# Kernel optimization log

Measured on AMD Instinct MI355X. Metric: run time of the kernel, lower is better.

## Reference

```python
import jax, jax.numpy as jnp
import numpy as np

E = 500000          # num edges
N = 50000           # num nodes
D_IN = 32           # n_input_features (edge feature dim)
D_HID = 128         # n_hidden_features
D_NODE = 16         # n_node_features; MLP head outputs D_NODE**2


def _linear_params(key, d_in, d_out):
    kw, kb = jax.random.split(key)
    bound = 1.0 / np.sqrt(d_in)
    W = jax.random.uniform(kw, (d_out, d_in), jnp.float32, -bound, bound)
    b = jax.random.uniform(kb, (d_out,), jnp.float32, -bound, bound)
    return W, b


def setup_inputs() -> dict:
    key = jax.random.key(0)
    k1, k2, k3, k4, k5, k6, k7 = jax.random.split(key, 7)
    edge_features = jax.random.normal(k1, (E, D_IN), jnp.float32)
    node_features = jax.random.normal(k2, (N, D_NODE), jnp.float32)
    edge_index = jax.random.randint(k3, (E, 2), 0, N, jnp.int64 if jax.config.jax_enable_x64 else jnp.int32)
    W1, b1 = _linear_params(k4, D_IN, D_HID)
    W2, b2 = _linear_params(k5, D_HID, D_HID)
    W3, b3 = _linear_params(k6, D_HID, D_HID)
    W4, b4 = _linear_params(k7, D_HID, D_NODE * D_NODE)
    return {
        "edge_features": edge_features,
        "node_features": node_features,
        "W1": W1, "b1": b1, "W2": W2, "b2": b2,
        "W3": W3, "b3": b3, "W4": W4, "b4": b4,
        "edge_index": edge_index,
    }


def reference(edge_features, node_features, W1, b1, W2, b2, W3, b3, W4, b4, edge_index):
    neighbors = edge_index[:, 1]                       # [E]
    ef = edge_features[neighbors]                      # [E, D_IN] gather
    nf = node_features[neighbors]                      # [E, D_NODE] gather
    h = jax.nn.relu(ef @ W1.T + b1)                    # [E, D_HID]
    h = jax.nn.relu(h @ W2.T + b2)
    h = jax.nn.relu(h @ W3.T + b3)
    edge_out = h @ W4.T + b4                           # [E, D_NODE**2]
    d = nf.shape[-1]
    message = edge_out.reshape(-1, d, d)               # [E, d, d]
    # per-edge matrix-vector product: (message @ nf[..., None]).squeeze(-1)
    return jnp.einsum("eij,ej->ei", message, nf)       # [E, d]
```

## Files before the change

### kernel.cpp

```cpp
#include <hip/hip_runtime.h>
#include <stdint.h>

typedef __attribute__((ext_vector_type(8))) short short8;
typedef __attribute__((ext_vector_type(4))) float f32x4;
typedef __attribute__((ext_vector_type(4))) unsigned int u32x4;

#define NE 500000
#define NN 50000
#define NTILES 3125
#define NPAIRS 1563

__device__ __forceinline__ unsigned int f2bf1(float f) {
  unsigned int u = __builtin_bit_cast(unsigned int, f);
  u += 0x7FFFu + ((u >> 16) & 1u);
  return u >> 16;
}
__device__ __forceinline__ unsigned int packbf2(float lo, float hi) {
  return f2bf1(lo) | (f2bf1(hi) << 16);
}
__device__ __forceinline__ short8 pack8(f32x4 a, f32x4 b) {
  short8 r;
  r[0] = (short)f2bf1(a[0]); r[1] = (short)f2bf1(a[1]);
  r[2] = (short)f2bf1(a[2]); r[3] = (short)f2bf1(a[3]);
  r[4] = (short)f2bf1(b[0]); r[5] = (short)f2bf1(b[1]);
  r[6] = (short)f2bf1(b[2]); r[7] = (short)f2bf1(b[3]);
  return r;
}

__global__ __launch_bounds__(512, 2) void mlp_kernel(
    const float* __restrict__ ef, const float* __restrict__ nfeat,
    const float* __restrict__ W1, const float* __restrict__ b1,
    const float* __restrict__ W2, const float* __restrict__ b2,
    const float* __restrict__ W3, const float* __restrict__ b3,
    const float* __restrict__ W4, const float* __restrict__ b4,
    float* __restrict__ Rout) {
  __shared__ __align__(16) unsigned short wlds[69632];
  __shared__ __align__(16) float blds[640];

  const int t = threadIdx.x;
  #pragma unroll
  for (int i = 0; i < 17; ++i) {
    int idx = t + i * 512;
    int f = idx >> 6, l = idx & 63;
    int c2 = l & 15, g = l >> 4;
    const float *pa, *pb;
    if (f < 8) {
      const float* base = W1 + (f * 16 + c2) * 32 + g * 8;
      pa = base; pb = base + 4;
    } else {
      const float* W; int i2, kfq, nb;
      if (f < 40)      { W = W2; i2 = f - 8;  kfq = i2 >> 3; nb = i2 & 7;  }
      else if (f < 72) { W = W3; i2 = f - 40; kfq = i2 >> 3; nb = i2 & 7;  }
      else             { W = W4; i2 = f - 72; kfq = i2 >> 4; nb = i2 & 15; }
      const float* base = W + (nb * 16 + c2) * 128 + g * 4;
      pa = base + kfq * 16;
      pb = base + (kfq + 4) * 16;
    }
    f32x4 x0 = *(const f32x4*)pa;
    f32x4 x1 = *(const f32x4*)pb;
    *(short8*)&wlds[f * 512 + l * 8] = pack8(x0, x1);
  }
  if (t < 160) {
    const float* s = t < 32 ? b1 + t * 4
                   : t < 64 ? b2 + (t - 32) * 4
                   : t < 96 ? b3 + (t - 64) * 4
                   :          b4 + (t - 96) * 4;
    ((f32x4*)blds)[t] = *(const f32x4*)s;
  }
  __syncthreads();

  const int lane = t & 63, w = t >> 6;
  const int l15 = lane & 15, lg = lane >> 4;

  const int p = blockIdx.x * 8 + w;
  if (p >= NPAIRS) return;
  const int tA = 2 * p, tB = 2 * p + 1;
  const bool actB = (tB < NTILES);
  const int nA = tA * 16, nB = (actB ? tB : tA) * 16;

  auto transition = [&](const f32x4* a, short8* af) {
    unsigned int pk[8][2];
    #pragma unroll
    for (int nb = 0; nb < 8; ++nb) {
      pk[nb][0] = packbf2(fmaxf(a[nb][0], 0.f), fmaxf(a[nb][1], 0.f));
      pk[nb][1] = packbf2(fmaxf(a[nb][2], 0.f), fmaxf(a[nb][3], 0.f));
    }
    #pragma unroll
    for (int kf = 0; kf < 4; ++kf) {
      u32x4 u = { pk[kf][0], pk[kf][1], pk[kf + 4][0], pk[kf + 4][1] };
      af[kf] = __builtin_bit_cast(short8, u);
    }
  };

  const float* xa = ef + (nA + l15) * 32 + lg * 8;
  const float* xb = ef + (nB + l15) * 32 + lg * 8;
  short8 a1A = pack8(*(const f32x4*)xa, *(const f32x4*)(xa + 4));
  short8 a1B = pack8(*(const f32x4*)xb, *(const f32x4*)(xb + 4));
  f32x4 accA[8], accB[8];
  #pragma unroll
  for (int nb = 0; nb < 8; ++nb) {
    f32x4 c0 = *(const f32x4*)&blds[nb * 16 + lg * 4];
    short8 wv = *(const short8*)&wlds[nb * 512 + lane * 8];
    accA[nb] = __builtin_amdgcn_mfma_f32_16x16x32_bf16(wv, a1A, c0, 0, 0, 0);
    accB[nb] = __builtin_amdgcn_mfma_f32_16x16x32_bf16(wv, a1B, c0, 0, 0, 0);
  }
  short8 afA[4], afB[4];
  transition(accA, afA);
  transition(accB, afB);

  #pragma unroll
  for (int L = 0; L < 2; ++L) {
    const int wbase = 8 + L * 32, bbase = 128 + L * 128;
    #pragma unroll
    for (int nb = 0; nb < 8; ++nb) {
      f32x4 c0 = *(const f32x4*)&blds[bbase + nb * 16 + lg * 4];
      f32x4 cA = c0, cB = c0;
      #pragma unroll
      for (int kf = 0; kf < 4; ++kf) {
        short8 wv = *(const short8*)&wlds[(wbase + kf * 8 + nb) * 512 + lane * 8];
        cA = __builtin_amdgcn_mfma_f32_16x16x32_bf16(wv, afA[kf], cA, 0, 0, 0);
        cB = __builtin_amdgcn_mfma_f32_16x16x32_bf16(wv, afB[kf], cB, 0, 0, 0);
      }
      accA[nb] = cA; accB[nb] = cB;
    }
    transition(accA, afA);
    transition(accB, afB);
  }

  f32x4 nfvA = *(const f32x4*)(nfeat + (nA + l15) * 16 + lg * 4);
  f32x4 nfvB = *(const f32x4*)(nfeat + (nB + l15) * 16 + lg * 4);
  float oA0 = 0.f, oA1 = 0.f, oA2 = 0.f, oA3 = 0.f;
  float oB0 = 0.f, oB1 = 0.f, oB2 = 0.f, oB3 = 0.f;
  #pragma unroll
  for (int nb = 0; nb < 16; ++nb) {
    f32x4 c0 = *(const f32x4*)&blds[384 + nb * 16 + lg * 4];
    f32x4 dA = c0, dB = c0;
    #pragma unroll
    for (int kf = 0; kf < 4; ++kf) {
      short8 wv = *(const short8*)&wlds[(72 + kf * 16 + nb) * 512 + lane * 8];
      dA = __builtin_amdgcn_mfma_f32_16x16x32_bf16(wv, afA[kf], dA, 0, 0, 0);
      dB = __builtin_amdgcn_mfma_f32_16x16x32_bf16(wv, afB[kf], dB, 0, 0, 0);
    }
    float pA = dA[0] * nfvA[0] + dA[1] * nfvA[1] + dA[2] * nfvA[2] + dA[3] * nfvA[3];
    float pB = dB[0] * nfvB[0] + dB[1] * nfvB[1] + dB[2] * nfvB[2] + dB[3] * nfvB[3];
    pA += __shfl_xor(pA, 16, 64); pA += __shfl_xor(pA, 32, 64);
    pB += __shfl_xor(pB, 16, 64); pB += __shfl_xor(pB, 32, 64);
    int rs = nb - lg * 4;
    oA0 = (rs == 0) ? pA : oA0; oA1 = (rs == 1) ? pA : oA1;
    oA2 = (rs == 2) ? pA : oA2; oA3 = (rs == 3) ? pA : oA3;
    oB0 = (rs == 0) ? pB : oB0; oB1 = (rs == 1) ? pB : oB1;
    oB2 = (rs == 2) ? pB : oB2; oB3 = (rs == 3) ? pB : oB3;
  }
  f32x4 oA = { oA0, oA1, oA2, oA3 };
  *(f32x4*)(Rout + (nA + l15) * 16 + lg * 4) = oA;
  if (actB) {
    f32x4 oB = { oB0, oB1, oB2, oB3 };
    *(f32x4*)(Rout + (nB + l15) * 16 + lg * 4) = oB;
  }
}

__global__ __launch_bounds__(256) void scatter_kernel(
    const int* __restrict__ eidx, const float* __restrict__ Rbuf,
    float* __restrict__ out) {
  int tid = blockIdx.x * 256 + threadIdx.x;
  const int total = NE * 4;
  const int stride = gridDim.x * 256;
  for (; tid < total; tid += stride) {
    int e = tid >> 2, p = tid & 3;
    int nb = eidx[2 * e + 1];
    f32x4 v = *(const f32x4*)(Rbuf + nb * 16 + p * 4);
    __builtin_nontemporal_store(v, (f32x4*)(out + e * 16 + p * 4));
  }
}

extern "C" void kernel_launch(void* const* d_in, const int* in_sizes, int n_in,
                              void* d_out, int out_size, void* d_ws, size_t ws_size,
                              hipStream_t stream) {
  const float* ef = (const float*)d_in[0];
  const float* nf = (const float*)d_in[1];
  const float* W1 = (const float*)d_in[2];
  const float* b1 = (const float*)d_in[3];
  const float* W2 = (const float*)d_in[4];
  const float* b2 = (const float*)d_in[5];
  const float* W3 = (const float*)d_in[6];
  const float* b3 = (const float*)d_in[7];
  const float* W4 = (const float*)d_in[8];
  const float* b4 = (const float*)d_in[9];
  const int* eidx = (const int*)d_in[10];

  float* Rbuf = (float*)d_ws;
  float* out = (float*)d_out;

  hipLaunchKernelGGL(mlp_kernel, dim3(256), dim3(512), 0, stream,
                     ef, nf, W1, b1, W2, b2, W3, b3, W4, b4, Rbuf);
  hipLaunchKernelGGL(scatter_kernel, dim3(2048), dim3(256), 0, stream, eidx, Rbuf, out);
}
```

Before: 36.28 us.

## Fuse MLP and scatter kernels into one cooperative launch with grid sync

Merges the per-node MLP kernel and the edge scatter kernel into a single cooperative kernel, separated by a threadfence and a grid-wide sync, to remove the second launch and the gap between kernels. The scatter phase now runs on 256x512 threads instead of 2048x256, using a 2x unrolled grid-stride loop. The cost is the cooperative launch overhead and the grid barrier. The scatter also gets fewer resident waves, since LDS use and launch bounds now limit occupancy for that phase.

```diff
diff --git a/kernel.cpp b/kernel.cpp
--- a/kernel.cpp
+++ b/kernel.cpp
@@ -1,5 +1,8 @@
 #include <hip/hip_runtime.h>
+#include <hip/hip_cooperative_groups.h>
 #include <stdint.h>
+
+namespace cg = cooperative_groups;
 
 typedef __attribute__((ext_vector_type(8))) short short8;
 typedef __attribute__((ext_vector_type(4))) float f32x4;
@@ -9,6 +12,8 @@
 #define NN 50000
 #define NTILES 3125
 #define NPAIRS 1563
+#define GRID_X 256
+#define BLOCK_X 512
 
 __device__ __forceinline__ unsigned int f2bf1(float f) {
   unsigned int u = __builtin_bit_cast(unsigned int, f);
@@ -27,149 +32,157 @@
   return r;
 }
 
-__global__ __launch_bounds__(512, 2) void mlp_kernel(
+__global__ __launch_bounds__(BLOCK_X, 2) void fused_kernel(
     const float* __restrict__ ef, const float* __restrict__ nfeat,
     const float* __restrict__ W1, const float* __restrict__ b1,
     const float* __restrict__ W2, const float* __restrict__ b2,
     const float* __restrict__ W3, const float* __restrict__ b3,
     const float* __restrict__ W4, const float* __restrict__ b4,
-    float* __restrict__ Rout) {
+    float* __restrict__ Rout,
+    const int* __restrict__ eidx, float* __restrict__ out) {
   __shared__ __align__(16) unsigned short wlds[69632];
   __shared__ __align__(16) float blds[640];
 
   const int t = threadIdx.x;
-  #pragma unroll
-  for (int i = 0; i < 17; ++i) {
-    int idx = t + i * 512;
-    int f = idx >> 6, l = idx & 63;
-    int c2 = l & 15, g = l >> 4;
-    const float *pa, *pb;
-    if (f < 8) {
-      const float* base = W1 + (f * 16 + c2) * 32 + g * 8;
-      pa = base; pb = base + 4;
-    } else {
-      const float* W; int i2, kfq, nb;
-      if (f < 40)      { W = W2; i2 = f - 8;  kfq = i2 >> 3; nb = i2 & 7;  }
-      else if (f < 72) { W = W3; i2 = f - 40; kfq = i2 >> 3; nb = i2 & 7;  }
-      else             { W = W4; i2 = f - 72; kfq = i2 >> 4; nb = i2 & 15; }
-      const float* base = W + (nb * 16 + c2) * 128 + g * 4;
-      pa = base + kfq * 16;
-      pb = base + (kfq + 4) * 16;
-    }
-    f32x4 x0 = *(const f32x4*)pa;
-    f32x4 x1 = *(const f32x4*)pb;
-    *(short8*)&wlds[f * 512 + l * 8] = pack8(x0, x1);
+  const bool block_has_work = (blockIdx.x * 8 < NPAIRS);
+
+  if (block_has_work) {
+    #pragma unroll
+    for (int i = 0; i < 17; ++i) {
+      int idx = t + i * 512;
+      int f = idx >> 6, l = idx & 63;
+      int c2 = l & 15, g = l >> 4;
+      const float *pa, *pb;
+      if (f < 8) {
+        const float* base = W1 + (f * 16 + c2) * 32 + g * 8;
+        pa = base; pb = base + 4;
+      } else {
+        const float* W; int i2, kfq, nb;
+        if (f < 40)      { W = W2; i2 = f - 8;  kfq = i2 >> 3; nb = i2 & 7;  }
+        else if (f < 72) { W = W3; i2 = f - 40; kfq = i2 >> 3; nb = i2 & 7;  }
+        else             { W = W4; i2 = f - 72; kfq = i2 >> 4; nb = i2 & 15; }
+        const float* base = W + (nb * 16 + c2) * 128 + g * 4;
+        pa = base + kfq * 16;
+        pb = base + (kfq + 4) * 16;
+      }
+      f32x4 x0 = *(const f32x4*)pa;
+      f32x4 x1 = *(const f32x4*)pb;
+      *(short8*)&wlds[f * 512 + l * 8] = pack8(x0, x1);
+    }
+    if (t < 160) {
+      const float* s = t < 32 ? b1 + t * 4
+                     : t < 64 ? b2 + (t - 32) * 4
+                     : t < 96 ? b3 + (t - 64) * 4
+                     :          b4 + (t - 96) * 4;
+      ((f32x4*)blds)[t] = *(const f32x4*)s;
+    }
+    __syncthreads();
+
+    const int lane = t & 63, w = t >> 6;
+    const int l15 = lane & 15, lg = lane >> 4;
+    const int p = blockIdx.x * 8 + w;
+
+    if (p < NPAIRS) {
+      const int tA = 2 * p, tB = 2 * p + 1;
+      const bool actB = (tB < NTILES);
+      const int nA = tA * 16, nB = (actB ? tB : tA) * 16;
+
+      auto transition = [&](const f32x4* a, short8* af) {
+        unsigned int pk[8][2];
+        #pragma unroll
+        for (int nb = 0; nb < 8; ++nb) {
+          pk[nb][0] = packbf2(fmaxf(a[nb][0], 0.f), fmaxf(a[nb][1], 0.f));
+          pk[nb][1] = packbf2(fmaxf(a[nb][2], 0.f), fmaxf(a[nb][3], 0.f));
+        }
+        #pragma unroll
+        for (int kf = 0; kf < 4; ++kf) {
+          u32x4 u = { pk[kf][0], pk[kf][1], pk[kf + 4][0], pk[kf + 4][1] };
+          af[kf] = __builtin_bit_cast(short8, u);
+        }
+      };
+
+      const float* xa = ef + (nA + l15) * 32 + lg * 8;
+      const float* xb = ef + (nB + l15) * 32 + lg * 8;
+      short8 a1A = pack8(*(const f32x4*)xa, *(const f32x4*)(xa + 4));
+      short8 a1B = pack8(*(const f32x4*)xb, *(const f32x4*)(xb + 4));
+      f32x4 accA[8], accB[8];
+      #pragma unroll
+      for (int nb = 0; nb < 8; ++nb) {
+        f32x4 c0 = *(const f32x4*)&blds[nb * 16 + lg * 4];
+        short8 wv = *(const short8*)&wlds[nb * 512 + lane * 8];
+        accA[nb] = __builtin_amdgcn_mfma_f32_16x16x32_bf16(wv, a1A, c0, 0, 0, 0);
+        accB[nb] = __builtin_amdgcn_mfma_f32_16x16x32_bf16(wv, a1B, c0, 0, 0, 0);
+      }
+      short8 afA[4], afB[4];
+      transition(accA, afA);
+      transition(accB, afB);
+
+      #pragma unroll
+      for (int L = 0; L < 2; ++L) {
+        const int wbase = 8 + L * 32, bbase = 128 + L * 128;
+        #pragma unroll
+        for (int nb = 0; nb < 8; ++nb) {
+          f32x4 c0 = *(const f32x4*)&blds[bbase + nb * 16 + lg * 4];
+          f32x4 cA = c0, cB = c0;
+          #pragma unroll
+          for (int kf = 0; kf < 4; ++kf) {
+            short8 wv = *(const short8*)&wlds[(wbase + kf * 8 + nb) * 512 + lane * 8];
+            cA = __builtin_amdgcn_mfma_f32_16x16x32_bf16(wv, afA[kf], cA, 0, 0, 0);
+            cB = __builtin_amdgcn_mfma_f32_16x16x32_bf16(wv, afB[kf], cB, 0, 0, 0);
+          }
+          accA[nb] = cA; accB[nb] = cB;
+        }
+        transition(accA, afA);
+        transition(accB, afB);
+      }
+
+      f32x4 nfvA = *(const f32x4*)(nfeat + (nA + l15) * 16 + lg * 4);
+      f32x4 nfvB = *(const f32x4*)(nfeat + (nB + l15) * 16 + lg * 4);
+      float oA0 = 0.f, oA1 = 0.f, oA2 = 0.f, oA3 = 0.f;
+      float oB0 = 0.f, oB1 = 0.f, oB2 = 0.f, oB3 = 0.f;
+      #pragma unroll
+      for (int nb = 0; nb < 16; ++nb) {
+        f32x4 c0 = *(const f32x4*)&blds[384 + nb * 16 + lg * 4];
+        f32x4 dA = c0, dB = c0;
+        #pragma unroll
+        for (int kf = 0; kf < 4; ++kf) {
+          short8 wv = *(const short8*)&wlds[(72 + kf * 16 + nb) * 512 + lane * 8];
+          dA = __builtin_amdgcn_mfma_f32_16x16x32_bf16(wv, afA[kf], dA, 0, 0, 0);
+          dB = __builtin_amdgcn_mfma_f32_16x16x32_bf16(wv, afB[kf], dB, 0, 0, 0);
+        }
+        float pA = dA[0]*nfvA[0] + dA[1]*nfvA[1] + dA[2]*nfvA[2] + dA[3]*nfvA[3];
+        float pB = dB[0]*nfvB[0] + dB[1]*nfvB[1] + dB[2]*nfvB[2] + dB[3]*nfvB[3];
+        pA += __shfl_xor(pA, 16, 64); pA += __shfl_xor(pA, 32, 64);
+        pB += __shfl_xor(pB, 16, 64); pB += __shfl_xor(pB, 32, 64);
+        int rs = nb - lg * 4;
+        oA0 = (rs == 0) ? pA : oA0; oA1 = (rs == 1) ? pA : oA1;
+        oA2 = (rs == 2) ? pA : oA2; oA3 = (rs == 3) ? pA : oA3;
+        oB0 = (rs == 0) ? pB : oB0; oB1 = (rs == 1) ? pB : oB1;
+        oB2 = (rs == 2) ? pB : oB2; oB3 = (rs == 3) ? pB : oB3;
+      }
+      f32x4 oA = { oA0, oA1, oA2, oA3 };
+      *(f32x4*)(Rout + (nA + l15) * 16 + lg * 4) = oA;
+      if (actB) {
+        f32x4 oB = { oB0, oB1, oB2, oB3 };
+        *(f32x4*)(Rout + (nB + l15) * 16 + lg * 4) = oB;
+      }
+    }
   }
-  if (t < 160) {
-    const float* s = t < 32 ? b1 + t * 4
-                   : t < 64 ? b2 + (t - 32) * 4
-                   : t < 96 ? b3 + (t - 64) * 4
-                   :          b4 + (t - 96) * 4;
-    ((f32x4*)blds)[t] = *(const f32x4*)s;
-  }
-  __syncthreads();
-
-  const int lane = t & 63, w = t >> 6;
-  const int l15 = lane & 15, lg = lane >> 4;
-
-  const int p = blockIdx.x * 8 + w;
-  if (p >= NPAIRS) return;
-  const int tA = 2 * p, tB = 2 * p + 1;
-  const bool actB = (tB < NTILES);
-  const int nA = tA * 16, nB = (actB ? tB : tA) * 16;
-
-  auto transition = [&](const f32x4* a, short8* af) {
-    unsigned int pk[8][2];
-    #pragma unroll
-    for (int nb = 0; nb < 8; ++nb) {
-      pk[nb][0] = packbf2(fmaxf(a[nb][0], 0.f), fmaxf(a[nb][1], 0.f));
-      pk[nb][1] = packbf2(fmaxf(a[nb][2], 0.f), fmaxf(a[nb][3], 0.f));
-    }
-    #pragma unroll
-    for (int kf = 0; kf < 4; ++kf) {
-      u32x4 u = { pk[kf][0], pk[kf][1], pk[kf + 4][0], pk[kf + 4][1] };
-      af[kf] = __builtin_bit_cast(short8, u);
-    }
-  };
-
-  const float* xa = ef + (nA + l15) * 32 + lg * 8;
-  const float* xb = ef + (nB + l15) * 32 + lg * 8;
-  short8 a1A = pack8(*(const f32x4*)xa, *(const f32x4*)(xa + 4));
-  short8 a1B = pack8(*(const f32x4*)xb, *(const f32x4*)(xb + 4));
-  f32x4 accA[8], accB[8];
-  #pragma unroll
-  for (int nb = 0; nb < 8; ++nb) {
-    f32x4 c0 = *(const f32x4*)&blds[nb * 16 + lg * 4];
-    short8 wv = *(const short8*)&wlds[nb * 512 + lane * 8];
-    accA[nb] = __builtin_amdgcn_mfma_f32_16x16x32_bf16(wv, a1A, c0, 0, 0, 0);
-    accB[nb] = __builtin_amdgcn_mfma_f32_16x16x32_bf16(wv, a1B, c0, 0, 0, 0);
-  }
-  short8 afA[4], afB[4];
-  transition(accA, afA);
-  transition(accB, afB);
-
-  #pragma unroll
-  for (int L = 0; L < 2; ++L) {
-    const int wbase = 8 + L * 32, bbase = 128 + L * 128;
-    #pragma unroll
-    for (int nb = 0; nb < 8; ++nb) {
-      f32x4 c0 = *(const f32x4*)&blds[bbase + nb * 16 + lg * 4];
-      f32x4 cA = c0, cB = c0;
-      #pragma unroll
-      for (int kf = 0; kf < 4; ++kf) {
-        short8 wv = *(const short8*)&wlds[(wbase + kf * 8 + nb) * 512 + lane * 8];
-        cA = __builtin_amdgcn_mfma_f32_16x16x32_bf16(wv, afA[kf], cA, 0, 0, 0);
-        cB = __builtin_amdgcn_mfma_f32_16x16x32_bf16(wv, afB[kf], cB, 0, 0, 0);
-      }
-      accA[nb] = cA; accB[nb] = cB;
-    }
-    transition(accA, afA);
-    transition(accB, afB);
-  }
-
-  f32x4 nfvA = *(const f32x4*)(nfeat + (nA + l15) * 16 + lg * 4);
-  f32x4 nfvB = *(const f32x4*)(nfeat + (nB + l15) * 16 + lg * 4);
-  float oA0 = 0.f, oA1 = 0.f, oA2 = 0.f, oA3 = 0.f;
-  float oB0 = 0.f, oB1 = 0.f, oB2 = 0.f, oB3 = 0.f;
-  #pragma unroll
-  for (int nb = 0; nb < 16; ++nb) {
-    f32x4 c0 = *(const f32x4*)&blds[384 + nb * 16 + lg * 4];
-    f32x4 dA = c0, dB = c0;
-    #pragma unroll
-    for (int kf = 0; kf < 4; ++kf) {
-      short8 wv = *(const short8*)&wlds[(72 + kf * 16 + nb) * 512 + lane * 8];
-      dA = __builtin_amdgcn_mfma_f32_16x16x32_bf16(wv, afA[kf], dA, 0, 0, 0);
-      dB = __builtin_amdgcn_mfma_f32_16x16x32_bf16(wv, afB[kf], dB, 0, 0, 0);
-    }
-    float pA = dA[0] * nfvA[0] + dA[1] * nfvA[1] + dA[2] * nfvA[2] + dA[3] * nfvA[3];
-    float pB = dB[0] * nfvB[0] + dB[1] * nfvB[1] + dB[2] * nfvB[2] + dB[3] * nfvB[3];
-    pA += __shfl_xor(pA, 16, 64); pA += __shfl_xor(pA, 32, 64);
-    pB += __shfl_xor(pB, 16, 64); pB += __shfl_xor(pB, 32, 64);
-    int rs = nb - lg * 4;
-    oA0 = (rs == 0) ? pA : oA0; oA1 = (rs == 1) ? pA : oA1;
-    oA2 = (rs == 2) ? pA : oA2; oA3 = (rs == 3) ? pA : oA3;
-    oB0 = (rs == 0) ? pB : oB0; oB1 = (rs == 1) ? pB : oB1;
-    oB2 = (rs == 2) ? pB : oB2; oB3 = (rs == 3) ? pB : oB3;
-  }
-  f32x4 oA = { oA0, oA1, oA2, oA3 };
-  *(f32x4*)(Rout + (nA + l15) * 16 + lg * 4) = oA;
-  if (actB) {
-    f32x4 oB = { oB0, oB1, oB2, oB3 };
-    *(f32x4*)(Rout + (nB + l15) * 16 + lg * 4) = oB;
-  }
-}
-
-__global__ __launch_bounds__(256) void scatter_kernel(
-    const int* __restrict__ eidx, const float* __restrict__ Rbuf,
-    float* __restrict__ out) {
-  int tid = blockIdx.x * 256 + threadIdx.x;
-  const int total = NE * 4;
-  const int stride = gridDim.x * 256;
-  for (; tid < total; tid += stride) {
-    int e = tid >> 2, p = tid & 3;
-    int nb = eidx[2 * e + 1];
-    f32x4 v = *(const f32x4*)(Rbuf + nb * 16 + p * 4);
-    __builtin_nontemporal_store(v, (f32x4*)(out + e * 16 + p * 4));
+
+  __threadfence();
+  cg::this_grid().sync();
+
+  {
+    const int total = NE * 4;
+    const int stride = GRID_X * BLOCK_X;
+    int tid = blockIdx.x * BLOCK_X + t;
+    #pragma unroll 2
+    for (; tid < total; tid += stride) {
+      int e = tid >> 2, pp = tid & 3;
+      int nb = eidx[2 * e + 1];
+      f32x4 v = *(const f32x4*)(Rout + nb * 16 + pp * 4);
+      __builtin_nontemporal_store(v, (f32x4*)(out + e * 16 + pp * 4));
+    }
   }
 }
 
@@ -191,7 +204,10 @@
   float* Rbuf = (float*)d_ws;
   float* out = (float*)d_out;
 
-  hipLaunchKernelGGL(mlp_kernel, dim3(256), dim3(512), 0, stream,
-                     ef, nf, W1, b1, W2, b2, W3, b3, W4, b4, Rbuf);
-  hipLaunchKernelGGL(scatter_kernel, dim3(2048), dim3(256), 0, stream, eidx, Rbuf, out);
-}
+  void* args[] = { (void*)&ef, (void*)&nf, (void*)&W1, (void*)&b1,
+                   (void*)&W2, (void*)&b2, (void*)&W3, (void*)&b3,
+                   (void*)&W4, (void*)&b4, (void*)&Rbuf,
+                   (void*)&eidx, (void*)&out };
+  hipLaunchCooperativeKernel((void*)fused_kernel, dim3(GRID_X), dim3(BLOCK_X),
+                             args, 0, stream);
+}
```

Measured after the change: 141.9 us. 291% more time.
